# Optimization experiments

Hardware: AMD Instinct MI355X
Metric: run time of the kernel (lower is better)

The kernel has to match this reference:

```python
import jax, jax.numpy as jnp
import numpy as np

D = 2048
H = 16
HD = D // H  # 128
EPS = 1e-6
SCALE = HD ** -0.5


def rms_norm(x, w):
    var = jnp.mean(jnp.square(x), axis=-1, keepdims=True)
    return x * jax.lax.rsqrt(var + EPS) * w


def setup_inputs() -> dict:
    key = jax.random.key(0)
    ks = jax.random.split(key, 16)
    std = D ** -0.5
    B, P, S = 2, 1024, 2048
    inp = {
        "vision_features": jax.random.normal(ks[0], (B, P, D), jnp.float32),
        "language_features": jax.random.normal(ks[1], (B, S, D), jnp.float32),
        "vision_pos_embed": jax.random.normal(ks[2], (1, 1024, D), jnp.float32) * 0.02,
        "text_pos_embed": jax.random.normal(ks[3], (1, 2048, D), jnp.float32) * 0.02,
        "vision_norm_w": jnp.ones((D,), jnp.float32),
        "language_norm_w": jnp.ones((D,), jnp.float32),
    }
    wnames = ["w_vq", "w_vk", "w_vv", "w_lq", "w_lk", "w_lv", "w_v2l", "w_l2v", "w_out"]
    for i, n in enumerate(wnames):
        inp[n] = jax.random.normal(ks[4 + i], (D, D), jnp.float32) * std  # [out, in]
    return inp


def reference(vision_features, language_features, vision_pos_embed, text_pos_embed,
              vision_norm_w, language_norm_w,
              w_vq, w_vk, w_vv, w_lq, w_lk, w_lv, w_v2l, w_l2v, w_out):
    B, P, _ = vision_features.shape
    S = language_features.shape[1]

    vf = vision_features + vision_pos_embed[:, :P, :]
    lf = language_features + text_pos_embed[:, :S, :]

    vn = rms_norm(vf, vision_norm_w)
    ln = rms_norm(lf, language_norm_w)

    def proj(x, w):  # x [B,T,D], w [D,D] (out,in) -> [B,H,T,HD]
        y = jnp.einsum('btd,ed->bte', x, w)
        return y.reshape(x.shape[0], x.shape[1], H, HD).transpose(0, 2, 1, 3)

    v_q = proj(vn, w_vq) * SCALE
    v_k = proj(vn, w_vk)
    v_v = proj(vn, w_vv)
    l_q = proj(ln, w_lq) * SCALE
    l_k = proj(ln, w_lk)
    l_v = proj(ln, w_lv)

    # vision -> language cross attention: [B,H,P,S]
    v2l_scores = jnp.einsum('bhpd,bhsd->bhps', v_q, l_k)
    v2l_attn = jax.nn.softmax(v2l_scores.astype(jnp.float32), axis=-1).astype(vf.dtype)
    v2l_out = jnp.einsum('bhps,bhsd->bhpd', v2l_attn, l_v)
    v2l_out = v2l_out.transpose(0, 2, 1, 3).reshape(B, P, D)
    v2l_out = jnp.einsum('bpd,ed->bpe', v2l_out, w_v2l)

    # language -> vision cross attention: [B,H,S,P]
    l2v_scores = jnp.einsum('bhsd,bhpd->bhsp', l_q, v_k)
    l2v_attn = jax.nn.softmax(l2v_scores.astype(jnp.float32), axis=-1).astype(lf.dtype)
    l2v_out = jnp.einsum('bhsp,bhpd->bhsd', l2v_attn, v_v)
    l2v_out = l2v_out.transpose(0, 2, 1, 3).reshape(B, S, D)
    l2v_out = jnp.einsum('bsd,ed->bse', l2v_out, w_l2v)

    vision_output = vf + v2l_out
    language_output = lf + l2v_out
    fused = jnp.concatenate([vision_output, language_output], axis=1)
    fused_output = jnp.einsum('btd,ed->bte', fused, w_out)

    return fused_output, vision_output, language_output, v2l_attn
```

## Files before the change

### kernel.cpp

```cpp
#include <hip/hip_runtime.h>
#include <hip/hip_bf16.h>


typedef __bf16 b8 __attribute__((ext_vector_type(8)));
typedef float f4 __attribute__((ext_vector_type(4)));
typedef float f16v __attribute__((ext_vector_type(16)));
typedef unsigned int uint32;

#define MFMA_16(a,b,c) __builtin_amdgcn_mfma_f32_16x16x32_bf16(a,b,c,0,0,0)
#define MFMA_32(a,b,c) __builtin_amdgcn_mfma_f32_32x32x16_bf16(a,b,c,0,0,0)

__device__ __forceinline__ ushort f2bf(float f){
  uint32 u = __float_as_uint(f);
  return (ushort)((u + 0x7FFFu + ((u >> 16) & 1u)) >> 16);
}

__device__ __forceinline__ void async16(const void* g, void* l){
  __builtin_amdgcn_global_load_lds(
      (__attribute__((address_space(1))) void*)(g),
      (__attribute__((address_space(3))) void*)(l), 16, 0, 0);
}

__device__ __forceinline__ uint32 cvtpk(float a, float b){
  uint32 r;
  asm("v_cvt_pk_bf16_f32 %0, %1, %2" : "=v"(r) : "v"(a), "v"(b));
  return r;
}

struct CastArgs { const float* s[6]; ushort* d[6]; float sc[6]; int nseg; };

__global__ __launch_bounds__(256)
void cast_k(CastArgs a){
  int n = a.nseg << 20;
  for (int i = blockIdx.x*blockDim.x + threadIdx.x; i < n; i += gridDim.x*blockDim.x){
    int seg = i >> 20, off = i & 1048575;
    float4 v = reinterpret_cast<const float4*>(a.s[seg])[off];
    float sc = a.sc[seg];
    ushort4 o;
    o.x = f2bf(v.x*sc); o.y = f2bf(v.y*sc); o.z = f2bf(v.z*sc); o.w = f2bf(v.w*sc);
    reinterpret_cast<ushort4*>(a.d[seg])[off] = o;
  }
}

__global__ __launch_bounds__(256)
void prep_k(const float* __restrict__ vfeat, const float* __restrict__ lfeat,
            const float* __restrict__ vpos, const float* __restrict__ lpos,
            const float* __restrict__ vw, const float* __restrict__ lw,
            float* __restrict__ vfo, float* __restrict__ lfo,
            ushort* __restrict__ vnb, ushort* __restrict__ lnb)
{
  const int row = blockIdx.x;
  const float *src, *pos, *w;
  float* fo; ushort* nb;
  if (row < 2048){
    src = vfeat + (size_t)row*2048; pos = vpos + (size_t)(row & 1023)*2048;
    w = vw; fo = vfo + (size_t)row*2048; nb = vnb + (size_t)row*2048;
  } else {
    int r = row - 2048;
    src = lfeat + (size_t)r*2048; pos = lpos + (size_t)(r & 2047)*2048;
    w = lw; fo = lfo + (size_t)r*2048; nb = lnb + (size_t)r*2048;
  }
  const int t = threadIdx.x;
  float4 a0 = reinterpret_cast<const float4*>(src)[t];
  float4 p0 = reinterpret_cast<const float4*>(pos)[t];
  float4 a1 = reinterpret_cast<const float4*>(src)[t+256];
  float4 p1 = reinterpret_cast<const float4*>(pos)[t+256];
  a0.x += p0.x; a0.y += p0.y; a0.z += p0.z; a0.w += p0.w;
  a1.x += p1.x; a1.y += p1.y; a1.z += p1.z; a1.w += p1.w;
  float ss = a0.x*a0.x + a0.y*a0.y + a0.z*a0.z + a0.w*a0.w
           + a1.x*a1.x + a1.y*a1.y + a1.z*a1.z + a1.w*a1.w;
  #pragma unroll
  for (int o = 32; o > 0; o >>= 1) ss += __shfl_xor(ss, o, 64);
  __shared__ float red[4];
  if ((t & 63) == 0) red[t >> 6] = ss;
  __syncthreads();
  float rs = rsqrtf((red[0]+red[1]+red[2]+red[3]) * (1.0f/2048.0f) + 1e-6f);
  reinterpret_cast<float4*>(fo)[t]     = a0;
  reinterpret_cast<float4*>(fo)[t+256] = a1;
  float4 w0 = reinterpret_cast<const float4*>(w)[t];
  float4 w1 = reinterpret_cast<const float4*>(w)[t+256];
  ushort4 o0, o1;
  o0.x = f2bf(a0.x*rs*w0.x); o0.y = f2bf(a0.y*rs*w0.y);
  o0.z = f2bf(a0.z*rs*w0.z); o0.w = f2bf(a0.w*rs*w0.w);
  o1.x = f2bf(a1.x*rs*w1.x); o1.y = f2bf(a1.y*rs*w1.y);
  o1.z = f2bf(a1.z*rs*w1.z); o1.w = f2bf(a1.w*rs*w1.w);
  reinterpret_cast<ushort4*>(nb)[t]     = o0;
  reinterpret_cast<ushort4*>(nb)[t+256] = o1;
}

template<int MODE>
__global__ __launch_bounds__(256, 3)
void gemm_k(const ushort* __restrict__ A, const ushort* __restrict__ A2,
            const ushort* __restrict__ W, ushort* __restrict__ OB,
            ushort* __restrict__ VT, float* __restrict__ OF, int logT)
{
  __shared__ __align__(16) ushort As[4096];
  __shared__ __align__(16) ushort Bs[4096];
  const int tid = threadIdx.x;
  const int l = tid & 63, wid = tid >> 6;
  const int wm = (wid >> 1) * 64, wn = (wid & 1) * 64;
  const int m0 = blockIdx.y * 128, n0 = blockIdx.x * 128;
  const int lr = l & 15, lk = l >> 4;
  f4 acc[4][4] = {};
  for (int kt = 0; kt < 2048; kt += 32) {
    #pragma unroll
    for (int i = 0; i < 2; ++i){
      int c = wid*64 + l + i*256;
      int row = c >> 2, kc = (c & 3) * 8;
      const ushort* ga = A + (size_t)(m0 + row)*2048 + kt + kc;
      async16(ga, &As[c*8]);
      async16(W + (size_t)(n0 + row)*2048 + kt + kc, &Bs[c*8]);
    }
    __syncthreads();
    b8 af[4], bfr[4];
    #pragma unroll
    for (int i = 0; i < 4; ++i)
      af[i] = *reinterpret_cast<const b8*>(&As[(wm + i*16 + lr)*32 + lk*8]);
    #pragma unroll
    for (int j = 0; j < 4; ++j)
      bfr[j] = *reinterpret_cast<const b8*>(&Bs[(wn + j*16 + lr)*32 + lk*8]);
    #pragma unroll
    for (int i = 0; i < 4; ++i)
      #pragma unroll
      for (int j = 0; j < 4; ++j)
        acc[i][j] = MFMA_16(af[i], bfr[j], acc[i][j]);
    __syncthreads();
  }
  #pragma unroll
  for (int i = 0; i < 4; ++i){
    int row0 = m0 + wm + i*16 + lk*4;
    #pragma unroll
    for (int j = 0; j < 4; ++j){
      int col = n0 + wn + j*16 + lr;
      #pragma unroll
      for (int r = 0; r < 4; ++r){
        size_t idx = (size_t)(row0 + r)*2048 + col;
        float v = acc[i][j][r] + OF[idx];
        OF[idx] = v;
        OB[idx] = f2bf(v);
      }
    }
  }
}

template<int MODE>
__global__ __launch_bounds__(512, 2)
void gemm8_k(const ushort* __restrict__ A, const ushort* __restrict__ A2,
             const ushort* __restrict__ W, ushort* __restrict__ OB,
             ushort* __restrict__ VT, float* __restrict__ OF, int logT)
{
  __shared__ __align__(16) ushort Ls[65536];
  const int tid = threadIdx.x;
  const int l = tid & 63, wid = tid >> 6;
  const int wmid = wid >> 2, wnid = wid & 3;
  const int lrow = l & 15, lg = l >> 4, lx = l & 7;

  const int nbx = gridDim.x;
  const int nwg = nbx * gridDim.y;
  const int wg  = blockIdx.y*nbx + blockIdx.x;
  const int swz = (wg & 7)*(nwg >> 3) + (wg >> 3);
  const int m0 = (swz / nbx) * 256, n0 = (swz % nbx) * 256;

  const ushort* srcA[2][2];
  const ushort* srcB[2][2];
  int ldsOff[2];
  #pragma unroll
  for (int i = 0; i < 2; ++i){
    int c = tid + i*512;
    int r = c >> 3, gs = c & 7;
    int scol = (gs ^ (r & 7)) * 8;
    ldsOff[i] = c * 8;
    #pragma unroll
    for (int hh = 0; hh < 2; ++hh){
      int growA = m0 + hh*128 + r;
      const ushort* pa;
      if constexpr (MODE == 2){
        int bb = (growA >= 3072) ? 1 : 0;
        int rr = growA - bb*3072;
        pa = (rr < 1024) ? (A  + (size_t)(bb*1024 + rr)*2048)
                         : (A2 + (size_t)(bb*2048 + rr - 1024)*2048);
      } else {
        pa = A + (size_t)growA*2048;
      }
      srcA[hh][i] = pa + scol;
      srcB[hh][i] = W + (size_t)(n0 + hh*128 + r)*2048 + scol;
    }
  }

  #define STA8(hh, tt) { int bo_ = ((tt)&1)*32768; _Pragma("unroll") \
    for (int i_ = 0; i_ < 2; ++i_) \
      async16(srcA[hh][i_] + (tt)*64, &Ls[bo_ + (hh)*8192 + ldsOff[i_]]); }
  #define STB8(hh, tt) { int bo_ = ((tt)&1)*32768; _Pragma("unroll") \
    for (int i_ = 0; i_ < 2; ++i_) \
      async16(srcB[hh][i_] + (tt)*64, &Ls[bo_ + 16384 + (hh)*8192 + ldsOff[i_]]); }

  const int aBase = wmid*8192 + lrow*64;
  const int bBase = 16384 + (wnid>>1)*8192 + (wnid&1)*4096 + lrow*64;
  int gsw[2];
  gsw[0] = ((0*4 + lg) ^ lx) * 8;
  gsw[1] = ((1*4 + lg) ^ lx) * 8;

  constexpr int NT = 32;
  STB8(0,0); STB8(1,0); STA8(0,0); STA8(1,0); STB8(0,1); STB8(1,1); STA8(0,1);
  asm volatile("s_waitcnt vmcnt(6)" ::: "memory");
  __builtin_amdgcn_s_barrier();

  f4 acc[8][4] = {};
  b8 afr[4][2], b0r[2][2], b1r[2][2];

  for (int t = 0; t < NT; ++t){
    const ushort* Lb = &Ls[(t & 1) * 32768];
    #pragma unroll
    for (int mi = 0; mi < 4; ++mi)
      #pragma unroll
      for (int kk = 0; kk < 2; ++kk)
        afr[mi][kk] = *reinterpret_cast<const b8*>(&Lb[aBase + mi*1024 + gsw[kk]]);
    #pragma unroll
    for (int nj = 0; nj < 2; ++nj)
      #pragma unroll
      for (int kk = 0; kk < 2; ++kk)
        b0r[nj][kk] = *reinterpret_cast<const b8*>(&Lb[bBase + nj*1024 + gsw[kk]]);
    if (t+1 < NT) STA8(1, t+1);
    __builtin_amdgcn_s_barrier();
    asm volatile("s_waitcnt lgkmcnt(0)" ::: "memory");
    __builtin_amdgcn_s_setprio(1);
    #pragma unroll
    for (int mi = 0; mi < 4; ++mi)
      #pragma unroll
      for (int nj = 0; nj < 2; ++nj)
        #pragma unroll
        for (int kk = 0; kk < 2; ++kk)
          acc[mi][nj] = MFMA_16(afr[mi][kk], b0r[nj][kk], acc[mi][nj]);
    __builtin_amdgcn_s_setprio(0);
    __builtin_amdgcn_s_barrier();
    #pragma unroll
    for (int nj = 0; nj < 2; ++nj)
      #pragma unroll
      for (int kk = 0; kk < 2; ++kk)
        b1r[nj][kk] = *reinterpret_cast<const b8*>(&Lb[bBase + (2+nj)*1024 + gsw[kk]]);
    __builtin_amdgcn_s_barrier();
    asm volatile("s_waitcnt lgkmcnt(0)" ::: "memory");
    __builtin_amdgcn_s_setprio(1);
    #pragma unroll
    for (int mi = 0; mi < 4; ++mi)
      #pragma unroll
      for (int nj = 0; nj < 2; ++nj)
        #pragma unroll
        for (int kk = 0; kk < 2; ++kk)
          acc[mi][2+nj] = MFMA_16(afr[mi][kk], b1r[nj][kk], acc[mi][2+nj]);
    __builtin_amdgcn_s_setprio(0);
    __builtin_amdgcn_s_barrier();
    #pragma unroll
    for (int mi = 0; mi < 4; ++mi)
      #pragma unroll
      for (int kk = 0; kk < 2; ++kk)
        afr[mi][kk] = *reinterpret_cast<const b8*>(&Lb[aBase + 4096 + mi*1024 + gsw[kk]]);
    if (t+2 < NT) STB8(0, t+2);
    __builtin_amdgcn_s_barrier();
    asm volatile("s_waitcnt lgkmcnt(0)" ::: "memory");
    __builtin_amdgcn_s_setprio(1);
    #pragma unroll
    for (int mi = 0; mi < 4; ++mi)
      #pragma unroll
      for (int nj = 0; nj < 2; ++nj)
        #pragma unroll
        for (int kk = 0; kk < 2; ++kk)
          acc[4+mi][nj] = MFMA_16(afr[mi][kk], b0r[nj][kk], acc[4+mi][nj]);
    __builtin_amdgcn_s_setprio(0);
    __builtin_amdgcn_s_barrier();
    if (t+2 < NT){ STB8(1, t+2); STA8(0, t+2); }
    __builtin_amdgcn_s_barrier();
    __builtin_amdgcn_s_setprio(1);
    #pragma unroll
    for (int mi = 0; mi < 4; ++mi)
      #pragma unroll
      for (int nj = 0; nj < 2; ++nj)
        #pragma unroll
        for (int kk = 0; kk < 2; ++kk)
          acc[4+mi][2+nj] = MFMA_16(afr[mi][kk], b1r[nj][kk], acc[4+mi][2+nj]);
    __builtin_amdgcn_s_setprio(0);
    if (t+2 < NT){ asm volatile("s_waitcnt vmcnt(6)" ::: "memory"); }
    else         { asm volatile("s_waitcnt vmcnt(0)" ::: "memory"); }
    __builtin_amdgcn_s_barrier();
  }

  #pragma unroll
  for (int mi = 0; mi < 8; ++mi){
    int row0 = m0 + wmid*128 + mi*16 + lg*4;
    #pragma unroll
    for (int nj = 0; nj < 4; ++nj){
      int col = n0 + wnid*64 + nj*16 + lrow;
      if constexpr (MODE == 0){
        if (col < 4096){
          #pragma unroll
          for (int r = 0; r < 4; ++r)
            OB[(size_t)(row0 + r)*4096 + col] = f2bf(acc[mi][nj][r]);
        } else {
          int d = col - 4096, hh = d >> 7, dd = d & 127;
          int bb = row0 >> logT;
          int t0 = row0 - (bb << logT);
          ushort4 pk;
          pk.x = f2bf(acc[mi][nj][0]); pk.y = f2bf(acc[mi][nj][1]);
          pk.z = f2bf(acc[mi][nj][2]); pk.w = f2bf(acc[mi][nj][3]);
          *reinterpret_cast<ushort4*>(
              &VT[(((size_t)(bb*16 + hh)*128 + dd) << logT) + t0]) = pk;
        }
      } else {
        #pragma unroll
        for (int r = 0; r < 4; ++r)
          OF[(size_t)(row0 + r)*2048 + col] = acc[mi][nj][r];
      }
    }
  }
  #undef STA8
  #undef STB8
}

template<int SKV, int WARPS, bool WA>
__global__ __launch_bounds__(WARPS*64, 2)
void attn_k(const ushort* __restrict__ qbuf, const ushort* __restrict__ kbuf,
            const ushort* __restrict__ vtb, float* __restrict__ attn,
            ushort* __restrict__ ctx, int TQ)
{
  constexpr int NT = SKV / 32;
  constexpr int NI = 512 / (WARPS*64);
  __shared__ __align__(16) ushort Ks[2][4096];
  __shared__ __align__(16) ushort Vs[2][4096];
  __shared__ __align__(16) float ast[WA ? WARPS*32*36 : 4];
  __shared__ float linv[WARPS*32];
  const int tid = threadIdx.x;
  const int l = tid & 63, wid = tid >> 6;
  const int hi = l >> 5, q = l & 31;
  const int b = blockIdx.z, h = blockIdx.y;
  const int q0 = blockIdx.x*(WARPS*32) + wid*32;
  const ushort* kbase = kbuf + (size_t)b*SKV*4096 + 2048 + h*128;
  const ushort* vbase = vtb + ((size_t)(b*16 + h))*128*SKV;

  b8 qf[8];
  {
    const ushort* qp = qbuf + (size_t)(b*TQ + q0 + q)*4096 + h*128 + hi*8;
    #pragma unroll
    for (int kd = 0; kd < 8; ++kd)
      qf[kd] = *reinterpret_cast<const b8*>(qp + kd*16);
  }

  #define STK(tt, bi) { int S0_ = (tt)*32; _Pragma("unroll") \
    for (int i_ = 0; i_ < NI; ++i_){ \
      int c_ = wid*64 + l + i_*(WARPS*64); int s_ = c_>>4, g_ = c_&15; \
      async16(kbase + (size_t)(S0_+s_)*4096 + (g_^(s_&15))*8, &Ks[bi][c_*8]); } }
  #define STV(tt, bi) { int S0_ = (tt)*32; _Pragma("unroll") \
    for (int i_ = 0; i_ < NI; ++i_){ \
      int c_ = wid*64 + l + i_*(WARPS*64); int d_ = c_>>2, g_ = c_&3; \
      async16(vbase + (size_t)d_*SKV + S0_ + (g_^(d_&3))*8, &Vs[bi][c_*8]); } }

  float mrun = -1e30f, lrun = 0.0f;
  STK(0, 0);
  for (int t = 0; t < NT; ++t){
    __syncthreads();
    if (t+1 < NT) STK(t+1, (t+1)&1);
    f16v s16 = {};
    #pragma unroll
    for (int kd = 0; kd < 8; ++kd){
      int gg = (kd*2 + hi) ^ (q & 15);
      b8 kf = *reinterpret_cast<const b8*>(&Ks[t&1][q*128 + gg*8]);
      s16 = MFMA_32(kf, qf[kd], s16);
    }
    float tm = s16[0];
    #pragma unroll
    for (int r = 1; r < 16; ++r) tm = fmaxf(tm, s16[r]);
    float mnew = fmaxf(mrun, tm);
    float sum = 0.f;
    #pragma unroll
    for (int r = 0; r < 16; ++r) sum += exp2f(s16[r] - mnew);
    lrun = lrun * exp2f(mrun - mnew) + sum;
    mrun = mnew;
  }
  {
    float mo = __shfl_xor(mrun, 32, 64);
    float lo = __shfl_xor(lrun, 32, 64);
    float mf = fmaxf(mrun, mo);
    lrun = lrun * exp2f(mrun - mf) + lo * exp2f(mo - mf);
    mrun = mf;
  }
  float invl = 1.0f / lrun;
  if (hi == 0) linv[wid*32 + q] = invl;
  __syncthreads();
  STK(0, 0); STV(0, 0);

  f16v O[4] = {};
  for (int t = 0; t < NT; ++t){
    __syncthreads();
    if (t+1 < NT){ STK(t+1, (t+1)&1); STV(t+1, (t+1)&1); }
    const int bi = t & 1;
    f16v s16 = {};
    #pragma unroll
    for (int kd = 0; kd < 8; ++kd){
      int gg = (kd*2 + hi) ^ (q & 15);
      b8 kf = *reinterpret_cast<const b8*>(&Ks[bi][q*128 + gg*8]);
      s16 = MFMA_32(kf, qf[kd], s16);
    }
    float e[16];
    #pragma unroll
    for (int r = 0; r < 16; ++r) e[r] = exp2f(s16[r] - mrun);
    if constexpr (WA){
      float* myt = &ast[wid*32*36];
      #pragma unroll
      for (int r = 0; r < 16; ++r){
        int sr = (r&3) + 8*(r>>2) + 4*hi;
        myt[q*36 + sr] = e[r] * invl;
      }
    }
    #pragma unroll
    for (int ks = 0; ks < 2; ++ks){
      const int base = ks*8;
      uint32 A0 = cvtpk(e[base+0], e[base+1]);
      uint32 A1 = cvtpk(e[base+2], e[base+3]);
      uint32 B0 = cvtpk(e[base+4], e[base+5]);
      uint32 B1 = cvtpk(e[base+6], e[base+7]);
      uint32 A0x = (uint32)__shfl_xor((int)A0, 32, 64);
      uint32 A1x = (uint32)__shfl_xor((int)A1, 32, 64);
      uint32 B0x = (uint32)__shfl_xor((int)B0, 32, 64);
      uint32 B1x = (uint32)__shfl_xor((int)B1, 32, 64);
      uint4 ww;
      ww.x = hi ? B0x : A0;
      ww.y = hi ? B1x : A1;
      ww.z = hi ? B0  : A0x;
      ww.w = hi ? B1  : A1x;
      b8 pa = __builtin_bit_cast(b8, ww);
      #pragma unroll
      for (int nb = 0; nb < 4; ++nb){
        int d = nb*32 + q;
        int gg2 = (ks*2 + hi) ^ (d & 3);
        b8 vfr = *reinterpret_cast<const b8*>(&Vs[bi][d*32 + gg2*8]);
        O[nb] = MFMA_32(pa, vfr, O[nb]);
      }
    }
    if constexpr (WA){
      const float* myt = &ast[wid*32*36];
      size_t abase = ((size_t)(b*16 + h)*TQ + q0) * SKV + t*32;
      #pragma unroll
      for (int it = 0; it < 4; ++it){
        int qq = (l >> 3) + it*8;
        float4 vv = *reinterpret_cast<const float4*>(&myt[qq*36 + (l&7)*4]);
        *reinterpret_cast<float4*>(&attn[abase + (size_t)qq*SKV + (l&7)*4]) = vv;
      }
    }
  }
  #pragma unroll
  for (int nb = 0; nb < 4; ++nb){
    #pragma unroll
    for (int r = 0; r < 16; ++r){
      int lq = (r&3) + 8*(r>>2) + 4*hi;
      float val = O[nb][r] * linv[wid*32 + lq];
      ctx[(size_t)(b*TQ + q0 + lq)*2048 + h*128 + nb*32 + q] = f2bf(val);
    }
  }
  #undef STK
  #undef STV
}

extern "C" void kernel_launch(void* const* d_in, const int* in_sizes, int n_in,
                              void* d_out, int out_size, void* d_ws, size_t ws_size,
                              hipStream_t stream)
{
  (void)in_sizes; (void)n_in; (void)out_size; (void)ws_size;
  const float* vfeat = (const float*)d_in[0];
  const float* lfeat = (const float*)d_in[1];
  const float* vpos  = (const float*)d_in[2];
  const float* lpos  = (const float*)d_in[3];
  const float* vw    = (const float*)d_in[4];
  const float* lw    = (const float*)d_in[5];
  const float* w_vq  = (const float*)d_in[6];
  const float* w_vk  = (const float*)d_in[7];
  const float* w_vv  = (const float*)d_in[8];
  const float* w_lq  = (const float*)d_in[9];
  const float* w_lk  = (const float*)d_in[10];
  const float* w_lv  = (const float*)d_in[11];
  const float* w_v2l = (const float*)d_in[12];
  const float* w_l2v = (const float*)d_in[13];
  const float* w_out = (const float*)d_in[14];

  float* out     = (float*)d_out;
  float* fused_o = out;
  float* vis_o   = out + 12582912;
  float* lan_o   = out + 16777216;
  float* attn_o  = out + 25165824;

  ushort* ws = (ushort*)d_ws;
  ushort* wcat_v = ws;
  ushort* wcat_l = wcat_v + 12582912;
  ushort* vnb    = wcat_l + 12582912;
  ushort* lnb    = vnb + 4194304;
  ushort* vqk    = lnb + 8388608;
  ushort* lqk    = vqk + 8388608;
  ushort* vtv    = lqk + 16777216;
  ushort* vtl    = vtv + 4194304;
  ushort* vctx    = wcat_v;
  ushort* lctx    = wcat_v + 4194304;
  ushort* w_v2l_b = wcat_l;
  ushort* w_l2v_b = wcat_l + 4194304;
  ushort* w_out_b = wcat_l + 8388608;

  const float QS = 0.08838834764831845f * 1.4426950408889634f;

  {
    CastArgs a;
    a.s[0]=w_vq; a.d[0]=wcat_v;           a.sc[0]=QS;
    a.s[1]=w_vk; a.d[1]=wcat_v+4194304;   a.sc[1]=1.f;
    a.s[2]=w_vv; a.d[2]=wcat_v+8388608;   a.sc[2]=1.f;
    a.s[3]=w_lq; a.d[3]=wcat_l;           a.sc[3]=QS;
    a.s[4]=w_lk; a.d[4]=wcat_l+4194304;   a.sc[4]=1.f;
    a.s[5]=w_lv; a.d[5]=wcat_l+8388608;   a.sc[5]=1.f;
    a.nseg = 6;
    cast_k<<<2048,256,0,stream>>>(a);
  }
  prep_k<<<6144,256,0,stream>>>(vfeat,lfeat,vpos,lpos,vw,lw,vis_o,lan_o,vnb,lnb);
  gemm8_k<0><<<dim3(24,8 ),512,0,stream>>>(vnb,nullptr,wcat_v,vqk,vtv,nullptr,10);
  gemm8_k<0><<<dim3(24,16),512,0,stream>>>(lnb,nullptr,wcat_l,lqk,vtl,nullptr,11);
  {
    CastArgs a;
    a.s[0]=w_v2l; a.d[0]=w_v2l_b; a.sc[0]=1.f;
    a.s[1]=w_l2v; a.d[1]=w_l2v_b; a.sc[1]=1.f;
    a.s[2]=w_out; a.d[2]=w_out_b; a.sc[2]=1.f;
    a.nseg = 3;
    cast_k<<<2048,256,0,stream>>>(a);
  }
  attn_k<2048,4,true ><<<dim3( 8,16,2),256,0,stream>>>(vqk,lqk,vtl,attn_o,vctx,1024);
  attn_k<1024,4,false><<<dim3(16,16,2),256,0,stream>>>(lqk,vqk,vtv,nullptr,lctx,2048);
  gemm_k<1><<<dim3(16,16),256,0,stream>>>(vctx,nullptr,w_v2l_b,vnb,nullptr,vis_o,0);
  gemm_k<1><<<dim3(16,32),256,0,stream>>>(lctx,nullptr,w_l2v_b,lnb,nullptr,lan_o,0);
  gemm8_k<2><<<dim3(8,24),512,0,stream>>>(vnb,lnb,w_out_b,nullptr,nullptr,fused_o,0);
}
```

Baseline: 1.181 ms.

## Merge vision and language GEMM launches into single grids over concatenated rows

The separate vision and language QKV projection GEMMs become one gemm8_k launch. Each workgroup picks its weight, output and V-transpose buffers from its row tile. The two context-projection GEMMs are likewise merged into one gemmc_k launch with a grouped block swizzle. The fused-output GEMM now maps concatenated rows with an index remap instead of two base pointers. The goal is fewer launches and better wave filling and tail behaviour, but it relies on the vision and language buffers (vnb/lnb, vctx/lctx) being contiguous in memory.

```diff
diff --git a/kernel.cpp b/kernel.cpp
--- a/kernel.cpp
+++ b/kernel.cpp
@@ -25,6 +25,10 @@
   uint32 r;
   asm("v_cvt_pk_bf16_f32 %0, %1, %2" : "=v"(r) : "v"(a), "v"(b));
   return r;
+}
+
+__device__ __forceinline__ int fconcat(int f){
+  return (f < 1024) ? f : (f < 3072) ? f + 1024 : (f < 4096) ? f - 2048 : f;
 }
 
 struct CastArgs { const float* s[6]; ushort* d[6]; float sc[6]; int nseg; };
@@ -88,18 +92,27 @@
   reinterpret_cast<ushort4*>(nb)[t+256] = o1;
 }
 
-template<int MODE>
 __global__ __launch_bounds__(256, 3)
-void gemm_k(const ushort* __restrict__ A, const ushort* __restrict__ A2,
-            const ushort* __restrict__ W, ushort* __restrict__ OB,
-            ushort* __restrict__ VT, float* __restrict__ OF, int logT)
+void gemmc_k(const ushort* __restrict__ A,
+             const ushort* __restrict__ Wv, const ushort* __restrict__ Wl,
+             ushort* __restrict__ OBv, ushort* __restrict__ OBl,
+             float* __restrict__ OFv, float* __restrict__ OFl)
 {
   __shared__ __align__(16) ushort As[4096];
   __shared__ __align__(16) ushort Bs[4096];
   const int tid = threadIdx.x;
   const int l = tid & 63, wid = tid >> 6;
   const int wm = (wid >> 1) * 64, wn = (wid & 1) * 64;
-  const int m0 = blockIdx.y * 128, n0 = blockIdx.x * 128;
+  const int wg = blockIdx.y*16 + blockIdx.x;
+  const int swz = (wg & 7)*96 + (wg >> 3);
+  const int byp = swz >> 4, bxp = swz & 15;
+  const bool lang = byp >= 16;
+  const int m0g = byp * 128;
+  const int m0l = (lang ? byp - 16 : byp) * 128;
+  const int n0 = bxp * 128;
+  const ushort* W = lang ? Wl : Wv;
+  ushort* OB = lang ? OBl : OBv;
+  float*  OF = lang ? OFl : OFv;
   const int lr = l & 15, lk = l >> 4;
   f4 acc[4][4] = {};
   for (int kt = 0; kt < 2048; kt += 32) {
@@ -107,8 +120,7 @@
     for (int i = 0; i < 2; ++i){
       int c = wid*64 + l + i*256;
       int row = c >> 2, kc = (c & 3) * 8;
-      const ushort* ga = A + (size_t)(m0 + row)*2048 + kt + kc;
-      async16(ga, &As[c*8]);
+      async16(A + (size_t)(m0g + row)*2048 + kt + kc, &As[c*8]);
       async16(W + (size_t)(n0 + row)*2048 + kt + kc, &Bs[c*8]);
     }
     __syncthreads();
@@ -128,7 +140,7 @@
   }
   #pragma unroll
   for (int i = 0; i < 4; ++i){
-    int row0 = m0 + wm + i*16 + lk*4;
+    int row0 = m0l + wm + i*16 + lk*4;
     #pragma unroll
     for (int j = 0; j < 4; ++j){
       int col = n0 + wn + j*16 + lr;
@@ -145,9 +157,11 @@
 
 template<int MODE>
 __global__ __launch_bounds__(512, 2)
-void gemm8_k(const ushort* __restrict__ A, const ushort* __restrict__ A2,
-             const ushort* __restrict__ W, ushort* __restrict__ OB,
-             ushort* __restrict__ VT, float* __restrict__ OF, int logT)
+void gemm8_k(const ushort* __restrict__ A,
+             const ushort* __restrict__ Wv, const ushort* __restrict__ Wl,
+             ushort* __restrict__ OBv, ushort* __restrict__ OBl,
+             ushort* __restrict__ VTv, ushort* __restrict__ VTl,
+             float* __restrict__ OF)
 {
   __shared__ __align__(16) ushort Ls[65536];
   const int tid = threadIdx.x;
@@ -159,7 +173,22 @@
   const int nwg = nbx * gridDim.y;
   const int wg  = blockIdx.y*nbx + blockIdx.x;
   const int swz = (wg & 7)*(nwg >> 3) + (wg >> 3);
-  const int m0 = (swz / nbx) * 256, n0 = (swz % nbx) * 256;
+  const int mt = swz / nbx, nt = swz % nbx;
+  const int n0 = nt * 256;
+  const int m0g = mt * 256;
+  const ushort* W;
+  ushort* OB; ushort* VT;
+  int logT, m0l;
+  if constexpr (MODE == 0){
+    const bool lang = mt >= 8;
+    W = lang ? Wl : Wv;
+    OB = lang ? OBl : OBv;
+    VT = lang ? VTl : VTv;
+    logT = lang ? 11 : 10;
+    m0l = lang ? (mt - 8)*256 : m0g;
+  } else {
+    W = Wv; OB = nullptr; VT = nullptr; logT = 0; m0l = m0g;
+  }
 
   const ushort* srcA[2][2];
   const ushort* srcB[2][2];
@@ -172,17 +201,9 @@
     ldsOff[i] = c * 8;
     #pragma unroll
     for (int hh = 0; hh < 2; ++hh){
-      int growA = m0 + hh*128 + r;
-      const ushort* pa;
-      if constexpr (MODE == 2){
-        int bb = (growA >= 3072) ? 1 : 0;
-        int rr = growA - bb*3072;
-        pa = (rr < 1024) ? (A  + (size_t)(bb*1024 + rr)*2048)
-                         : (A2 + (size_t)(bb*2048 + rr - 1024)*2048);
-      } else {
-        pa = A + (size_t)growA*2048;
-      }
-      srcA[hh][i] = pa + scol;
+      int growA = m0g + hh*128 + r;
+      if constexpr (MODE == 2) growA = fconcat(growA);
+      srcA[hh][i] = A + (size_t)growA*2048 + scol;
       srcB[hh][i] = W + (size_t)(n0 + hh*128 + r)*2048 + scol;
     }
   }
@@ -286,7 +307,7 @@
 
   #pragma unroll
   for (int mi = 0; mi < 8; ++mi){
-    int row0 = m0 + wmid*128 + mi*16 + lg*4;
+    int row0 = m0l + wmid*128 + mi*16 + lg*4;
     #pragma unroll
     for (int nj = 0; nj < 4; ++nj){
       int col = n0 + wnid*64 + nj*16 + lrow;
@@ -515,8 +536,8 @@
     cast_k<<<2048,256,0,stream>>>(a);
   }
   prep_k<<<6144,256,0,stream>>>(vfeat,lfeat,vpos,lpos,vw,lw,vis_o,lan_o,vnb,lnb);
-  gemm8_k<0><<<dim3(24,8 ),512,0,stream>>>(vnb,nullptr,wcat_v,vqk,vtv,nullptr,10);
-  gemm8_k<0><<<dim3(24,16),512,0,stream>>>(lnb,nullptr,wcat_l,lqk,vtl,nullptr,11);
+  gemm8_k<0><<<dim3(24,24),512,0,stream>>>(vnb, wcat_v, wcat_l,
+                                           vqk, lqk, vtv, vtl, nullptr);
   {
     CastArgs a;
     a.s[0]=w_v2l; a.d[0]=w_v2l_b; a.sc[0]=1.f;
@@ -527,7 +548,8 @@
   }
   attn_k<2048,4,true ><<<dim3( 8,16,2),256,0,stream>>>(vqk,lqk,vtl,attn_o,vctx,1024);
   attn_k<1024,4,false><<<dim3(16,16,2),256,0,stream>>>(lqk,vqk,vtv,nullptr,lctx,2048);
-  gemm_k<1><<<dim3(16,16),256,0,stream>>>(vctx,nullptr,w_v2l_b,vnb,nullptr,vis_o,0);
-  gemm_k<1><<<dim3(16,32),256,0,stream>>>(lctx,nullptr,w_l2v_b,lnb,nullptr,lan_o,0);
-  gemm8_k<2><<<dim3(8,24),512,0,stream>>>(vnb,lnb,w_out_b,nullptr,nullptr,fused_o,0);
-}
+  gemmc_k<<<dim3(16,48),256,0,stream>>>(vctx, w_v2l_b, w_l2v_b,
+                                        vnb, lnb, vis_o, lan_o);
+  gemm8_k<2><<<dim3(8,24),512,0,stream>>>(vnb, w_out_b, nullptr,
+                                          nullptr, nullptr, nullptr, nullptr, fused_o);
+}
```

Measured after the change: 1.108 ms. -6.2%, faster.
